# Optimization experiments

Measured on AMD Instinct MI355X. Metric: run time of the kernel, lower is better.

The kernel has to match this reference:

```python
import jax, jax.numpy as jnp
import numpy as np
from jax.ops import segment_sum

N_NODES = 50000
N_EDGES = 800000
N_GRAPHS = 64
N_CLASSES = 100
HEADS = 5
EPS = 1e-5


def _self_loops(edge_index, n):
    loop = jnp.arange(n, dtype=edge_index.dtype)
    src = jnp.concatenate([edge_index[0], loop])
    dst = jnp.concatenate([edge_index[1], loop])
    return src, dst


def gcn_conv(x, src, dst, n, w, b):
    xw = x @ w  # [N, C]
    deg = segment_sum(jnp.ones_like(dst, dtype=xw.dtype), dst, num_segments=n)
    dis = jnp.where(deg > 0, jax.lax.rsqrt(jnp.maximum(deg, 1.0)), 0.0)
    norm = dis[src] * dis[dst]  # [E']
    out = segment_sum(norm[:, None] * xw[src], dst, num_segments=n)
    return out + b


def batch_norm(x, gamma, beta):
    mu = jnp.mean(x, axis=0)
    var = jnp.var(x, axis=0)
    return (x - mu) * jax.lax.rsqrt(var + EPS) * gamma + beta


def gcn_block(x, src, dst, n, w, b, gamma, beta, residual):
    h = jax.nn.gelu(batch_norm(gcn_conv(x, src, dst, n, w, b), gamma, beta), approximate=False)
    return h + x if residual else h


def gat_conv(x, src, dst, n, w, att_src, att_dst, bias):
    H, C = att_src.shape
    xw = (x @ w).reshape(n, H, C)  # [N,H,C]
    a_src = jnp.sum(xw * att_src, axis=-1)  # [N,H]
    a_dst = jnp.sum(xw * att_dst, axis=-1)  # [N,H]
    e = jax.nn.leaky_relu(a_src[src] + a_dst[dst], 0.2)  # [E',H]
    m = jax.ops.segment_max(e, dst, num_segments=n)
    alpha = jnp.exp(e - m[dst])
    denom = segment_sum(alpha, dst, num_segments=n)
    alpha = alpha / jnp.maximum(denom[dst], 1e-16)
    # loop over small fixed head count to bound memory of [E',C] gathers
    outs = []
    for h in range(H):
        msg = alpha[:, h:h + 1] * xw[src, h, :]  # [E',C]
        outs.append(segment_sum(msg, dst, num_segments=n))
    out = jnp.mean(jnp.stack(outs, axis=0), axis=0)  # concat=False -> mean over heads
    return out + bias


def graph_layer_norm(x, gamma, beta):
    # PyG LayerNorm(mode='graph') with batch=None: normalize over all nodes+features
    mu = jnp.mean(x)
    var = jnp.var(x)
    return (x - mu) * jax.lax.rsqrt(var + EPS) * gamma + beta


def layer_norm(x, gamma, beta):
    mu = jnp.mean(x, axis=-1, keepdims=True)
    var = jnp.var(x, axis=-1, keepdims=True)
    return (x - mu) * jax.lax.rsqrt(var + EPS) * gamma + beta


def global_mean_pool(x, batch, n_graphs):
    sums = segment_sum(x, batch, num_segments=n_graphs)
    cnt = segment_sum(jnp.ones((x.shape[0],), x.dtype), batch, num_segments=n_graphs)
    return sums / jnp.maximum(cnt, 1.0)[:, None]


def setup_inputs() -> dict:
    key = jax.random.key(0)
    ks = jax.random.split(key, 24)
    glorot = lambda k, shp: jax.random.normal(k, shp, jnp.float32) * np.sqrt(2.0 / (shp[0] + shp[-1]))
    inp = {}
    inp['x'] = jax.random.normal(ks[0], (N_NODES, 3), jnp.float32)
    inp['edge_index'] = jax.random.randint(ks[1], (2, N_EDGES), 0, N_NODES, jnp.int64)
    inp['batch'] = jnp.sort(jax.random.randint(ks[2], (N_NODES,), 0, N_GRAPHS, jnp.int64))
    # input block 3->128
    inp['w_in'] = glorot(ks[3], (3, 128)); inp['b_in'] = jnp.zeros((128,), jnp.float32)
    inp['g_in'] = jnp.ones((128,), jnp.float32); inp['be_in'] = jnp.zeros((128,), jnp.float32)
    # hidden block 128->128 (n_hidden_blocks=2 -> one hidden block)
    inp['w_h'] = glorot(ks[4], (128, 128)); inp['b_h'] = jnp.zeros((128,), jnp.float32)
    inp['g_h'] = jnp.ones((128,), jnp.float32); inp['be_h'] = jnp.zeros((128,), jnp.float32)
    # GAT 128 -> 5 heads x 128, mean
    inp['w_gat'] = glorot(ks[5], (128, HEADS * 128))
    inp['att_src'] = glorot(ks[6], (HEADS, 128)); inp['att_dst'] = glorot(ks[7], (HEADS, 128))
    inp['b_gat'] = jnp.zeros((128,), jnp.float32)
    # output block 128->512
    inp['w_out'] = glorot(ks[8], (128, 512)); inp['b_out'] = jnp.zeros((512,), jnp.float32)
    inp['g_out'] = jnp.ones((512,), jnp.float32); inp['be_out'] = jnp.zeros((512,), jnp.float32)
    # encoder layer norm
    inp['g_ln'] = jnp.ones((512,), jnp.float32); inp['be_ln'] = jnp.zeros((512,), jnp.float32)
    # projection head
    inp['w_p1'] = glorot(ks[9], (512, 128)); inp['b_p1'] = jnp.zeros((128,), jnp.float32)
    inp['g_pbn'] = jnp.ones((128,), jnp.float32); inp['be_pbn'] = jnp.zeros((128,), jnp.float32)
    inp['w_p2'] = glorot(ks[10], (128, 128)); inp['b_p2'] = jnp.zeros((128,), jnp.float32)
    inp['g_pln'] = jnp.ones((128,), jnp.float32); inp['be_pln'] = jnp.zeros((128,), jnp.float32)
    # classifier
    inp['w_c'] = glorot(ks[11], (128, N_CLASSES)); inp['b_c'] = jnp.zeros((N_CLASSES,), jnp.float32)
    return inp


def reference(x, edge_index, batch, w_in, b_in, g_in, be_in, w_h, b_h, g_h, be_h,
              w_gat, att_src, att_dst, b_gat, w_out, b_out, g_out, be_out,
              g_ln, be_ln, w_p1, b_p1, g_pbn, be_pbn, w_p2, b_p2, g_pln, be_pln,
              w_c, b_c):
    n = x.shape[0]
    src, dst = _self_loops(edge_index, n)
    # encoder
    h = gcn_block(x, src, dst, n, w_in, b_in, g_in, be_in, residual=False)
    h = gcn_block(h, src, dst, n, w_h, b_h, g_h, be_h, residual=True)
    h = gat_conv(h, src, dst, n, w_gat, att_src, att_dst, b_gat)
    h = gcn_block(h, src, dst, n, w_out, b_out, g_out, be_out, residual=False)
    h = graph_layer_norm(h, g_ln, be_ln)
    h = global_mean_pool(h, batch, N_GRAPHS)  # [G,512]
    # projection head
    p = jax.nn.gelu(batch_norm(h @ w_p1 + b_p1, g_pbn, be_pbn), approximate=False)
    p = layer_norm(p @ w_p2 + b_p2 + p, g_pln, be_pln)
    # normalize + classifier
    x1 = p / jnp.maximum(jnp.linalg.norm(p, axis=1, keepdims=True), 1e-12)
    c1 = jax.nn.log_softmax(x1 @ w_c + b_c, axis=1)
    return (x1, c1)
```

## Files before the change

kernel.cpp:

```cpp
#include <hip/hip_runtime.h>
#include <hip/hip_bf16.h>
#include <math.h>

#define NN 50000
#define NE 800000
#define NG 64
#define NC 100
#define EPSV 1e-5f
#define PBN 256
#define SCB 196
#define SPL 8
#define PRB 128

typedef unsigned int   u32;
typedef unsigned short u16;
typedef __attribute__((ext_vector_type(8))) short bf16x8;
typedef __attribute__((ext_vector_type(4))) float f32x4;

__device__ __forceinline__ float gelu_f(float x){
  return 0.5f*x*(1.0f + erff(x*0.70710678118654752f));
}
__device__ __forceinline__ float bf2f(u16 u){
  return __uint_as_float(((u32)u)<<16);
}
__device__ __forceinline__ float2 bf2f2(u32 u){
  float2 r;
  r.x = __uint_as_float(u<<16);
  r.y = __uint_as_float(u & 0xffff0000u);
  return r;
}
__device__ __forceinline__ u16 f2bf(float f){
  __hip_bfloat16 h = __float2bfloat16(f);
  return *(u16*)&h;
}
__device__ __forceinline__ u32 pack_bf2(float a, float b){
  return (u32)f2bf(a) | ((u32)f2bf(b)<<16);
}

__global__ void k_deg_init(int* deg){
  int i = blockIdx.x*256 + threadIdx.x;
  if (i < NN) deg[i] = 1;
}
__global__ void k_deg_hist(const int* ei, int* deg){
  int e = blockIdx.x*256 + threadIdx.x;
  if (e < NE) atomicAdd(&deg[ei[NE + e]], 1);
}
__global__ void k_dis(const int* deg, float* dis){
  int i = blockIdx.x*256 + threadIdx.x;
  if (i < NN) dis[i] = rsqrtf((float)deg[i]);
}
__global__ void k_scanA(const int* deg, int* bsum){
  __shared__ int red[256];
  int b = blockIdx.x, t = threadIdx.x;
  int i = b*256 + t;
  red[t] = (i < NN) ? deg[i]-1 : 0;
  __syncthreads();
  for (int st = 128; st; st >>= 1){
    if (t < st) red[t] += red[t+st];
    __syncthreads();
  }
  if (t == 0) bsum[b] = red[0];
}
__global__ void k_scanB(const int* bsum, int* boff){
  __shared__ int sh[256];
  int t = threadIdx.x;
  sh[t] = (t < SCB) ? bsum[t] : 0;
  __syncthreads();
  for (int d = 1; d < 256; d <<= 1){
    int v = (t >= d) ? sh[t-d] : 0;
    __syncthreads();
    sh[t] += v;
    __syncthreads();
  }
  if (t == 0) boff[0] = 0;
  if (t < SCB) boff[t+1] = sh[t];
}
__global__ void k_scanC(const int* deg, const int* boff, int* off, int* cur){
  __shared__ int sh[256];
  int b = blockIdx.x, t = threadIdx.x;
  int i = b*256 + t;
  int v = (i < NN) ? deg[i]-1 : 0;
  sh[t] = v;
  __syncthreads();
  for (int d = 1; d < 256; d <<= 1){
    int u = (t >= d) ? sh[t-d] : 0;
    __syncthreads();
    sh[t] += u;
    __syncthreads();
  }
  if (i < NN){
    int excl = boff[b] + sh[t] - v;
    off[i] = excl; cur[i] = excl;
    if (i == NN-1) off[NN] = boff[b] + sh[t];
  }
}
__global__ void k_scatter(const int* ei, int* cur, int* col){
  int e = blockIdx.x*256 + threadIdx.x;
  if (e < NE){
    int s = ei[e], d = ei[NE + e];
    int p = atomicAdd(&cur[d], 1);
    col[p] = s;
  }
}

__global__ void k_agg3(const float* x, const int* off, const int* col,
                       const float* dis, float* aggx){
  int i = blockIdx.x*256 + threadIdx.x;
  if (i >= NN) return;
  float di = dis[i];
  float w0 = di*di;
  float a0 = w0*x[i*3], a1 = w0*x[i*3+1], a2 = w0*x[i*3+2];
  int lo = off[i], hi = off[i+1];
  for (int e = lo; e < hi; ++e){
    int s = col[e];
    float w = dis[s]*di;
    a0 += w*x[s*3]; a1 += w*x[s*3+1]; a2 += w*x[s*3+2];
  }
  aggx[i*3] = a0; aggx[i*3+1] = a1; aggx[i*3+2] = a2;
}

__global__ void k_mm_in(const float* aggx, const float* w, const float* bias, u32* outp){
  int gid = blockIdx.x*256 + threadIdx.x;
  if (gid >= NN*64) return;
  int i = gid >> 6, j2 = (gid & 63)*2;
  float a = aggx[i*3]*w[j2]   + aggx[i*3+1]*w[128+j2]   + aggx[i*3+2]*w[256+j2]   + bias[j2];
  float b = aggx[i*3]*w[j2+1] + aggx[i*3+1]*w[128+j2+1] + aggx[i*3+2]*w[256+j2+1] + bias[j2+1];
  outp[gid] = pack_bf2(a, b);
}

__global__ void k_prepB(const float* B, int ldB, int K, int ncc, u16* Bf){
  int gid = blockIdx.x*256 + threadIdx.x;
  int tot = ncc*K*128;
  if (gid >= tot) return;
  int cc = gid / (K*128);
  int rem = gid - cc*(K*128);
  int k = rem >> 7, n = rem & 127;
  int c128 = k >> 7, kk = k & 127;
  int nt = n >> 4, i = n & 15;
  int ks = kk >> 5, jg = (kk >> 3) & 3, e = kk & 7;
  size_t addr = (size_t)cc*K*128 +
                ((((size_t)(c128*8 + nt)*4 + ks)*4 + jg)*16 + i)*8 + e;
  Bf[addr] = f2bf(B[(size_t)k*ldB + cc*128 + n]);
}
__global__ void k_prepBG(const float* w_gat, u16* Bf){
  int gid = blockIdx.x*256 + threadIdx.x;
  if (gid >= 640*128) return;
  int k = gid >> 7, n = gid & 127;
  int h = k >> 7, kk = k & 127;
  int nt = n >> 4, i = n & 15;
  int ks = kk >> 5, jg = (kk >> 3) & 3, e = kk & 7;
  size_t addr = ((((size_t)(h*8 + nt)*4 + ks)*4 + jg)*16 + i)*8 + e;
  Bf[addr] = f2bf(0.2f * w_gat[(size_t)kk*640 + h*128 + n]);
}

__global__ __launch_bounds__(256) void k_mm_mfma(const u16* A, int lda, int M, int K,
                        const u16* Bf, u16* C, int ldC, const float* bias){
  __shared__ u16 ct[64*132];
  int tid = threadIdx.x;
  int w = tid >> 6, l = tid & 63;
  int jg = l >> 4, ii = l & 15;
  int m0 = blockIdx.x*64 + w*16;
  int cc = blockIdx.y;
  int arow = m0 + ii; if (arow >= M) arow = M-1;
  const u16* Bfc = Bf + (size_t)cc*K*128;
  f32x4 acc[8] = {};
  for (int c128 = 0; c128 < (K >> 7); ++c128){
    const u16* Ar = A + (size_t)arow*lda + c128*128;
    bf16x8 af[4];
    #pragma unroll
    for (int ks = 0; ks < 4; ++ks)
      af[ks] = *(const bf16x8*)(Ar + ks*32 + jg*8);
    #pragma unroll
    for (int nt = 0; nt < 8; ++nt){
      f32x4 a4 = acc[nt];
      #pragma unroll
      for (int ks = 0; ks < 4; ++ks){
        bf16x8 bfr = *(const bf16x8*)(Bfc +
            ((((size_t)(c128*8 + nt)*4 + ks)*4 + jg)*16 + ii)*8);
        a4 = __builtin_amdgcn_mfma_f32_16x16x32_bf16(af[ks], bfr, a4, 0, 0, 0);
      }
      acc[nt] = a4;
    }
  }
  int cOut = cc*128;
  int lrow0 = w*16 + jg*4;
  #pragma unroll
  for (int nt = 0; nt < 8; ++nt){
    float bv = bias[cOut + nt*16 + ii];
    #pragma unroll
    for (int r = 0; r < 4; ++r)
      ct[(lrow0 + r)*132 + nt*16 + ii] = f2bf(acc[nt][r] + bv);
  }
  __syncthreads();
  int lr0 = tid >> 6;
  int lc = tid & 63;
  #pragma unroll
  for (int rr = 0; rr < 16; ++rr){
    int lrow = rr*4 + lr0;
    int grow = blockIdx.x*64 + lrow;
    if (grow < M)
      *(u32*)(C + (size_t)grow*ldC + cOut + lc*2) = *(const u32*)(ct + lrow*132 + lc*2);
  }
}

__global__ void k_gcn_agg64(const u16* xw, const int* off, const int* col,
                            const float* dis, u16* out){
  int i = blockIdx.x, t = threadIdx.x;
  float di = dis[i];
  float2 sv = bf2f2(((const u32*)(xw + (size_t)i*128))[t]);
  float w0 = di*di;
  float ax = w0*sv.x, ay = w0*sv.y;
  int lo = off[i], hi = off[i+1];
  int e = lo;
  for (; e + 4 <= hi; e += 4){
    int s0 = col[e], s1 = col[e+1], s2 = col[e+2], s3 = col[e+3];
    float wA = dis[s0]*di, wB = dis[s1]*di, wC = dis[s2]*di, wD = dis[s3]*di;
    float2 r0 = bf2f2(((const u32*)(xw + (size_t)s0*128))[t]);
    float2 r1 = bf2f2(((const u32*)(xw + (size_t)s1*128))[t]);
    float2 r2 = bf2f2(((const u32*)(xw + (size_t)s2*128))[t]);
    float2 r3 = bf2f2(((const u32*)(xw + (size_t)s3*128))[t]);
    ax += wA*r0.x; ay += wA*r0.y;
    ax += wB*r1.x; ay += wB*r1.y;
    ax += wC*r2.x; ay += wC*r2.y;
    ax += wD*r3.x; ay += wD*r3.y;
  }
  for (; e < hi; ++e){
    int s = col[e];
    float w = dis[s]*di;
    float2 rv = bf2f2(((const u32*)(xw + (size_t)s*128))[t]);
    ax += w*rv.x; ay += w*rv.y;
  }
  ((u32*)(out + (size_t)i*128))[t] = pack_bf2(ax, ay);
}

__global__ void k_bn_part(const u16* x, int stride, int W, float* part){
  __shared__ float shs[8][132];
  __shared__ float shq[8][132];
  int t = threadIdx.x;
  int ft = t & 31, rl = t >> 5;
  int f0 = ft*4;
  int fbase = blockIdx.x*128;
  int p = blockIdx.y;
  float s0=0.f,s1=0.f,s2=0.f,s3=0.f, q0=0.f,q1=0.f,q2=0.f,q3=0.f;
  for (int r = p + PBN*rl; r < NN; r += PBN*8){
    ushort4 u = *(const ushort4*)(x + (size_t)r*stride + fbase + f0);
    float v0 = bf2f(u.x), v1 = bf2f(u.y), v2 = bf2f(u.z), v3 = bf2f(u.w);
    s0 += v0; s1 += v1; s2 += v2; s3 += v3;
    q0 += v0*v0; q1 += v1*v1; q2 += v2*v2; q3 += v3*v3;
  }
  shs[rl][f0] = s0; shs[rl][f0+1] = s1; shs[rl][f0+2] = s2; shs[rl][f0+3] = s3;
  shq[rl][f0] = q0; shq[rl][f0+1] = q1; shq[rl][f0+2] = q2; shq[rl][f0+3] = q3;
  __syncthreads();
  if (t < 128){
    float s = 0.f, q = 0.f;
    #pragma unroll
    for (int r = 0; r < 8; ++r){ s += shs[r][t]; q += shq[r][t]; }
    size_t fb = (size_t)(fbase + t)*2*PBN;
    part[fb + p] = s;
    part[fb + PBN + p] = q;
  }
}
__global__ void k_bn_fin(const float* part, const float* g, const float* be,
                         float* ss, int W, float invn){
  __shared__ float rs[256], rq[256];
  int f = blockIdx.x, t = threadIdx.x;
  size_t fb = (size_t)f*2*PBN;
  rs[t] = part[fb + t];
  rq[t] = part[fb + PBN + t];
  __syncthreads();
  for (int st = 128; st; st >>= 1){
    if (t < st){ rs[t] += rs[t+st]; rq[t] += rq[t+st]; }
    __syncthreads();
  }
  if (t == 0){
    float mean = rs[0]*invn;
    float var  = rq[0]*invn - mean*mean;
    float sc = g[f]*rsqrtf(var + EPSV);
    ss[f] = sc;
    ss[W+f] = be[f] - mean*sc;
  }
}
template<bool RES>
__global__ void k_bn_apply(const u32* x, const float* ss, const u32* res, u32* out){
  const int n = NN*64;
  for (int idx = blockIdx.x*256 + threadIdx.x; idx < n; idx += gridDim.x*256){
    int f2 = (idx & 63)*2;
    float2 v = bf2f2(x[idx]);
    v.x = gelu_f(v.x*ss[f2]   + ss[128+f2]);
    v.y = gelu_f(v.y*ss[f2+1] + ss[128+f2+1]);
    if (RES){ float2 r = bf2f2(res[idx]); v.x += r.x; v.y += r.y; }
    out[idx] = pack_bf2(v.x, v.y);
  }
}

__global__ void k_wv(const float* w_gat, const float* att_s, const float* att_d,
                     float* wvs, float* wvd){
  int h = blockIdx.x, c = threadIdx.x;
  float ss = 0.f, sd = 0.f;
  const float* wr = w_gat + (size_t)c*640 + h*128;
  const float* as = att_s + h*128;
  const float* ad = att_d + h*128;
  for (int k = 0; k < 128; ++k){
    float wv = wr[k];
    ss += wv*as[k]; sd += wv*ad[k];
  }
  wvs[h*128+c] = ss; wvd[h*128+c] = sd;
}

__global__ void k_score10(const u16* h2, const float* wvs, const float* wvd,
                          float* asrc, float* adst){
  int i = blockIdx.x, t = threadIdx.x;
  float2 v = bf2f2(((const u32*)(h2 + (size_t)i*128))[t]);
  int f2 = 2*t;
  #pragma unroll
  for (int h = 0; h < 5; ++h){
    float vs = v.x*wvs[h*128+f2] + v.y*wvs[h*128+f2+1];
    float vd = v.x*wvd[h*128+f2] + v.y*wvd[h*128+f2+1];
    #pragma unroll
    for (int d = 32; d; d >>= 1){ vs += __shfl_xor(vs, d); vd += __shfl_xor(vd, d); }
    if (t == 0){ asrc[i*5+h] = vs; adst[i*5+h] = vd; }
  }
}

__global__ void k_prep5(const float* asrc, const float* adst,
                        const int* off, const int* col,
                        u16* sv, float* aself5, float* invb5){
  int i = blockIdx.x, t = threadIdx.x;
  int lo = off[i], hi = off[i+1];
  float ad[5], dn[5];
  #pragma unroll
  for (int h = 0; h < 5; ++h){ ad[h] = adst[i*5+h]; dn[h] = 0.f; }
  for (int e = lo + t; e < hi; e += 64){
    int s = col[e];
    u16 nb[5];
    #pragma unroll
    for (int h = 0; h < 5; ++h){
      float v = asrc[s*5+h] + ad[h];
      v = (v > 0.f) ? v : 0.2f*v;
      float ex = expf(v);
      u16 qq = f2bf(ex);
      nb[h] = qq;
      dn[h] += bf2f(qq);
    }
    uint4 pk;
    pk.x = (u32)nb[0] | ((u32)nb[1] << 16);
    pk.y = (u32)nb[2] | ((u32)nb[3] << 16);
    pk.z = (u32)nb[4];
    pk.w = 0;
    *(uint4*)(sv + (size_t)e*8) = pk;
  }
  #pragma unroll
  for (int h = 0; h < 5; ++h)
    #pragma unroll
    for (int d = 32; d; d >>= 1) dn[h] += __shfl_xor(dn[h], d);
  if (t == 0){
    #pragma unroll
    for (int h = 0; h < 5; ++h){
      float es = asrc[i*5+h] + ad[h];
      es = (es > 0.f) ? es : 0.2f*es;
      float esf = expf(es);
      aself5[i*5+h] = esf;
      invb5[i*5+h] = 1.f/fmaxf(dn[h] + esf, 1e-16f);
    }
  }
}

__global__ void k_gather5(const u16* h2, const int* off, const int* col,
                          const u16* sv, const float* aself5, const float* invb5,
                          u16* agg5){
  int i = blockIdx.x, t = threadIdx.x;
  float2 svv = bf2f2(((const u32*)(h2 + (size_t)i*128))[t]);
  float ax[5], ay[5];
  #pragma unroll
  for (int h = 0; h < 5; ++h){
    float a = aself5[i*5+h];
    ax[h] = a*svv.x; ay[h] = a*svv.y;
  }
  int lo = off[i], hi = off[i+1];
  int e = lo;
  for (; e + 2 <= hi; e += 2){
    int s0 = col[e], s1 = col[e+1];
    uint4 p0 = *(const uint4*)(sv + (size_t)e*8);
    uint4 p1 = *(const uint4*)(sv + (size_t)(e+1)*8);
    float2 r0 = bf2f2(((const u32*)(h2 + (size_t)s0*128))[t]);
    float2 r1 = bf2f2(((const u32*)(h2 + (size_t)s1*128))[t]);
    float a00 = bf2f((u16)(p0.x & 0xffff)), a01 = bf2f((u16)(p0.x >> 16));
    float a02 = bf2f((u16)(p0.y & 0xffff)), a03 = bf2f((u16)(p0.y >> 16));
    float a04 = bf2f((u16)(p0.z & 0xffff));
    float a10 = bf2f((u16)(p1.x & 0xffff)), a11 = bf2f((u16)(p1.x >> 16));
    float a12 = bf2f((u16)(p1.y & 0xffff)), a13 = bf2f((u16)(p1.y >> 16));
    float a14 = bf2f((u16)(p1.z & 0xffff));
    ax[0] += a00*r0.x + a10*r1.x; ay[0] += a00*r0.y + a10*r1.y;
    ax[1] += a01*r0.x + a11*r1.x; ay[1] += a01*r0.y + a11*r1.y;
    ax[2] += a02*r0.x + a12*r1.x; ay[2] += a02*r0.y + a12*r1.y;
    ax[3] += a03*r0.x + a13*r1.x; ay[3] += a03*r0.y + a13*r1.y;
    ax[4] += a04*r0.x + a14*r1.x; ay[4] += a04*r0.y + a14*r1.y;
  }
  for (; e < hi; ++e){
    int s = col[e];
    uint4 pk = *(const uint4*)(sv + (size_t)e*8);
    float2 rv = bf2f2(((const u32*)(h2 + (size_t)s*128))[t]);
    float a0 = bf2f((u16)(pk.x & 0xffff)), a1 = bf2f((u16)(pk.x >> 16));
    float a2 = bf2f((u16)(pk.y & 0xffff)), a3 = bf2f((u16)(pk.y >> 16));
    float a4 = bf2f((u16)(pk.z & 0xffff));
    ax[0] += a0*rv.x; ay[0] += a0*rv.y;
    ax[1] += a1*rv.x; ay[1] += a1*rv.y;
    ax[2] += a2*rv.x; ay[2] += a2*rv.y;
    ax[3] += a3*rv.x; ay[3] += a3*rv.y;
    ax[4] += a4*rv.x; ay[4] += a4*rv.y;
  }
  #pragma unroll
  for (int h = 0; h < 5; ++h){
    float iv = invb5[i*5+h];
    ((u32*)(agg5 + (size_t)i*640 + h*128))[t] = pack_bf2(ax[h]*iv, ay[h]*iv);
  }
}

__global__ void k_gstart(const int* batch, int* gs){
  int g = threadIdx.x;
  if (g > NG) return;
  int lo = 0, hi = NN;
  while (lo < hi){ int mid = (lo+hi) >> 1; if (batch[mid] < g) lo = mid+1; else hi = mid; }
  gs[g] = lo;
}
__global__ void k_poolstat(const u16* a512, const float* ss, const int* gs,
                           float* poolpart, float* sqpart){
  __shared__ float4 red4[512];
  __shared__ float redq[512];
  int g = blockIdx.x, sp = blockIdx.y, t = threadIdx.x;
  int ft = t & 127, rl = t >> 7;
  int f0 = ft*4;
  int lo = gs[g], hi = gs[g+1];
  float sc0 = ss[f0],     sc1 = ss[f0+1],     sc2 = ss[f0+2],     sc3 = ss[f0+3];
  float sh0 = ss[512+f0], sh1 = ss[512+f0+1], sh2 = ss[512+f0+2], sh3 = ss[512+f0+3];
  float4 s4 = {0.f,0.f,0.f,0.f};
  float q = 0.f;
  for (int r = lo + sp*4 + rl; r < hi; r += SPL*4){
    ushort4 u = *(const ushort4*)(a512 + (size_t)r*512 + f0);
    float v0 = gelu_f(bf2f(u.x)*sc0 + sh0);
    float v1 = gelu_f(bf2f(u.y)*sc1 + sh1);
    float v2 = gelu_f(bf2f(u.z)*sc2 + sh2);
    float v3 = gelu_f(bf2f(u.w)*sc3 + sh3);
    s4.x += v0; s4.y += v1; s4.z += v2; s4.w += v3;
    q += v0*v0 + v1*v1 + v2*v2 + v3*v3;
  }
  red4[t] = s4; redq[t] = q;
  __syncthreads();
  for (int st = 256; st; st >>= 1){
    if (t < st) redq[t] += redq[t+st];
    __syncthreads();
  }
  if (t == 0) sqpart[g*SPL + sp] = redq[0];
  if (rl == 0){
    float4 a = red4[t], b = red4[t+128], c = red4[t+256], d = red4[t+384];
    float4 o;
    o.x = a.x+b.x+c.x+d.x; o.y = a.y+b.y+c.y+d.y;
    o.z = a.z+b.z+c.z+d.z; o.w = a.w+b.w+c.w+d.w;
    ((float4*)poolpart)[((size_t)(g*SPL + sp))*128 + ft] = o;
  }
}
__global__ void k_poolredA(const float* poolpart, const float* sqpart,
                           float* ppred, float* sqred){
  __shared__ float rs_[256], rq_[256];
  int b = blockIdx.x, t = threadIdx.x;
  float s = 0.f, q = 0.f;
  const int tot = NG*SPL*512;
  for (int i = b*256 + t; i < tot; i += PRB*256) s += poolpart[i];
  for (int i = b*256 + t; i < NG*SPL; i += PRB*256) q += sqpart[i];
  rs_[t] = s; rq_[t] = q;
  __syncthreads();
  for (int st = 128; st; st >>= 1){
    if (t < st){ rs_[t] += rs_[t+st]; rq_[t] += rq_[t+st]; }
    __syncthreads();
  }
  if (t == 0){ ppred[b] = rs_[0]; sqred[b] = rq_[0]; }
}
__global__ void k_poolredB(const float* ppred, const float* sqred, float* scal){
  __shared__ float rs_[128], rq_[128];
  int t = threadIdx.x;
  rs_[t] = ppred[t]; rq_[t] = sqred[t];
  __syncthreads();
  for (int st = 64; st; st >>= 1){
    if (t < st){ rs_[t] += rs_[t+st]; rq_[t] += rq_[t+st]; }
    __syncthreads();
  }
  if (t == 0){
    float invn = 1.f/((float)NN*512.f);
    float mu  = rs_[0]*invn;
    float var = rq_[0]*invn - mu*mu;
    scal[2] = mu;
    scal[3] = rsqrtf(var + EPSV);
  }
}
__global__ void k_poolapply(const float* poolpart, const int* gs, const float* scal,
                            const float* gam, const float* bet, float* pooled){
  int g = blockIdx.x, f = threadIdx.x;
  float s = 0.f;
  #pragma unroll
  for (int sp = 0; sp < SPL; ++sp)
    s += poolpart[((size_t)(g*SPL + sp))*512 + f];
  float cnt = (float)max(gs[g+1] - gs[g], 1);
  pooled[g*512 + f] = (s/cnt - scal[2])*scal[3]*gam[f] + bet[f];
}

__global__ void k_head_mm1(const float* pooled, const float* w, const float* b, float* q){
  int g = blockIdx.x, j = threadIdx.x;
  float s = b[j];
  const float* pr = pooled + g*512;
  for (int k = 0; k < 512; ++k) s += pr[k]*w[k*128+j];
  q[g*128+j] = s;
}
__global__ void k_head_bn(const float* qin, const float* g_, const float* be_, float* qout){
  int f = threadIdx.x;
  float s = 0.f, sq = 0.f;
  for (int r = 0; r < NG; ++r){ float v = qin[r*128+f]; s += v; sq += v*v; }
  float mu = s*(1.f/NG), var = sq*(1.f/NG) - mu*mu;
  float sc = g_[f]*rsqrtf(var + EPSV);
  float sh = be_[f] - mu*sc;
  for (int r = 0; r < NG; ++r) qout[r*128+f] = gelu_f(qin[r*128+f]*sc + sh);
}
__global__ void k_head2c(const float* q2, const float* w, const float* b,
                         const float* gam, const float* bet,
                         const float* wc, const float* bc, float* out){
  int g = blockIdx.x, j = threadIdx.x;
  __shared__ float row[128], red[128], shv[3];
  row[j] = q2[g*128+j];
  __syncthreads();
  float s = b[j] + row[j];
  for (int k = 0; k < 128; ++k) s += row[k]*w[k*128+j];
  red[j] = s; __syncthreads();
  for (int st = 64; st; st >>= 1){ if (j < st) red[j] += red[j+st]; __syncthreads(); }
  if (j == 0) shv[0] = red[0]*(1.f/128.f);
  __syncthreads();
  float d = s - shv[0];
  red[j] = d*d; __syncthreads();
  for (int st = 64; st; st >>= 1){ if (j < st) red[j] += red[j+st]; __syncthreads(); }
  if (j == 0) shv[1] = rsqrtf(red[0]*(1.f/128.f) + EPSV);
  __syncthreads();
  float v = d*shv[1]*gam[j] + bet[j];
  red[j] = v*v; __syncthreads();
  for (int st = 64; st; st >>= 1){ if (j < st) red[j] += red[j+st]; __syncthreads(); }
  if (j == 0) shv[2] = 1.f/fmaxf(sqrtf(red[0]), 1e-12f);
  __syncthreads();
  float o = v*shv[2];
  out[g*128+j] = o;
  __syncthreads();
  row[j] = o;
  __syncthreads();
  float cs = -1e30f;
  if (j < NC){
    cs = bc[j];
    for (int k = 0; k < 128; ++k) cs += row[k]*wc[k*NC+j];
  }
  red[j] = cs; __syncthreads();
  for (int st = 64; st; st >>= 1){ if (j < st) red[j] = fmaxf(red[j], red[j+st]); __syncthreads(); }
  if (j == 0) shv[0] = red[0];
  __syncthreads();
  float e = (j < NC) ? expf(cs - shv[0]) : 0.f;
  red[j] = e; __syncthreads();
  for (int st = 64; st; st >>= 1){ if (j < st) red[j] += red[j+st]; __syncthreads(); }
  if (j == 0) shv[1] = logf(red[0]);
  __syncthreads();
  if (j < NC) out[NG*128 + g*NC+j] = cs - shv[0] - shv[1];
}

extern "C" void kernel_launch(void* const* d_in, const int* in_sizes, int n_in,
                              void* d_out, int out_size, void* d_ws, size_t ws_size,
                              hipStream_t stream){
  const float* x      = (const float*)d_in[0];
  const int*   ei     = (const int*)d_in[1];
  const int*   batch  = (const int*)d_in[2];
  const float* w_in   = (const float*)d_in[3];
  const float* b_in   = (const float*)d_in[4];
  const float* g_in   = (const float*)d_in[5];
  const float* be_in  = (const float*)d_in[6];
  const float* w_h    = (const float*)d_in[7];
  const float* b_h    = (const float*)d_in[8];
  const float* g_h    = (const float*)d_in[9];
  const float* be_h   = (const float*)d_in[10];
  const float* w_gat  = (const float*)d_in[11];
  const float* att_s  = (const float*)d_in[12];
  const float* att_d  = (const float*)d_in[13];
  const float* b_gat  = (const float*)d_in[14];
  const float* w_out  = (const float*)d_in[15];
  const float* b_out  = (const float*)d_in[16];
  const float* g_out  = (const float*)d_in[17];
  const float* be_out = (const float*)d_in[18];
  const float* g_ln   = (const float*)d_in[19];
  const float* be_ln  = (const float*)d_in[20];
  const float* w_p1   = (const float*)d_in[21];
  const float* b_p1   = (const float*)d_in[22];
  const float* g_pbn  = (const float*)d_in[23];
  const float* be_pbn = (const float*)d_in[24];
  const float* w_p2   = (const float*)d_in[25];
  const float* b_p2   = (const float*)d_in[26];
  const float* g_pln  = (const float*)d_in[27];
  const float* be_pln = (const float*)d_in[28];
  const float* w_c    = (const float*)d_in[29];
  const float* b_c    = (const float*)d_in[30];
  float* out = (float*)d_out;

  char* ws = (char*)d_ws;
  size_t o = 0;
  auto carve = [&](size_t bytes) -> char* {
    char* p = ws + o;
    o += (bytes + 255) & ~(size_t)255;
    return p;
  };
  int*   deg    = (int*)  carve((size_t)NN*4);
  int*   off    = (int*)  carve((size_t)(NN+1)*4);
  int*   cur    = (int*)  carve((size_t)NN*4);
  int*   col    = (int*)  carve((size_t)NE*4);
  float* dis    = (float*)carve((size_t)NN*4);
  int*   bsum   = (int*)  carve((size_t)SCB*4);
  int*   boff   = (int*)  carve((size_t)(SCB+1)*4);
  float* aggx3  = (float*)carve((size_t)NN*3*4);
  u16*   F0     = (u16*)  carve((size_t)NN*128*2);
  u16*   F1     = (u16*)  carve((size_t)NN*128*2);
  u16*   F2     = (u16*)  carve((size_t)NN*128*2);
  u16*   AGG5   = (u16*)  carve((size_t)NN*640*2);
  float* asrc   = (float*)carve((size_t)NN*5*4);
  float* adst   = (float*)carve((size_t)NN*5*4);
  float* aself5 = (float*)carve((size_t)NN*5*4);
  float* invb5  = (float*)carve((size_t)NN*5*4);
  float* wvs    = (float*)carve(640*4);
  float* wvd    = (float*)carve(640*4);
  u16*   BfH    = (u16*)  carve((size_t)128*128*2);
  u16*   BfG    = (u16*)  carve((size_t)640*128*2);
  u16*   BfO    = (u16*)  carve((size_t)128*512*2);
  float* part   = (float*)carve((size_t)512*2*PBN*4);
  float* poolpart = (float*)carve((size_t)NG*SPL*512*4);
  float* sqpart = (float*)carve((size_t)NG*SPL*4);
  float* ppred  = (float*)carve((size_t)PRB*4);
  float* sqred  = (float*)carve((size_t)PRB*4);
  float* ssbuf  = (float*)carve(1024*4);
  float* scal   = (float*)carve(64);
  int*   gst    = (int*)  carve(65*4);
  float* pooled = (float*)carve((size_t)NG*512*4);
  float* q      = (float*)carve((size_t)NG*128*4);
  float* q2     = (float*)carve((size_t)NG*128*4);
  if (o > ws_size) return;

  u16* A512 = AGG5;
  u16* sv   = F2;

  k_deg_init<<<196,256,0,stream>>>(deg);
  k_deg_hist<<<3125,256,0,stream>>>(ei, deg);
  k_dis<<<196,256,0,stream>>>(deg, dis);
  k_scanA<<<SCB,256,0,stream>>>(deg, bsum);
  k_scanB<<<1,256,0,stream>>>(bsum, boff);
  k_scanC<<<SCB,256,0,stream>>>(deg, boff, off, cur);
  k_scatter<<<3125,256,0,stream>>>(ei, cur, col);

  k_prepB<<<64,256,0,stream>>>(w_h, 128, 128, 1, BfH);
  k_prepBG<<<320,256,0,stream>>>(w_gat, BfG);
  k_prepB<<<256,256,0,stream>>>(w_out, 512, 128, 4, BfO);

  k_agg3<<<196,256,0,stream>>>(x, off, col, dis, aggx3);
  k_mm_in<<<(NN*64+255)/256,256,0,stream>>>(aggx3, w_in, b_in, (u32*)F0);
  k_bn_part<<<dim3(1,PBN),256,0,stream>>>(F0, 128, 128, part);
  k_bn_fin<<<128,256,0,stream>>>(part, g_in, be_in, ssbuf, 128, 1.f/NN);
  k_bn_apply<false><<<2048,256,0,stream>>>((u32*)F0, ssbuf, nullptr, (u32*)F1);

  k_gcn_agg64<<<NN,64,0,stream>>>(F1, off, col, dis, F0);
  k_mm_mfma<<<dim3(782,1),256,0,stream>>>(F0, 128, NN, 128, BfH, F2, 128, b_h);
  k_bn_part<<<dim3(1,PBN),256,0,stream>>>(F2, 128, 128, part);
  k_bn_fin<<<128,256,0,stream>>>(part, g_h, be_h, ssbuf, 128, 1.f/NN);
  k_bn_apply<true><<<2048,256,0,stream>>>((u32*)F2, ssbuf, (u32*)F1, (u32*)F0);

  k_wv<<<5,128,0,stream>>>(w_gat, att_s, att_d, wvs, wvd);
  k_score10<<<NN,64,0,stream>>>(F0, wvs, wvd, asrc, adst);
  k_prep5<<<NN,64,0,stream>>>(asrc, adst, off, col, sv, aself5, invb5);
  k_gather5<<<NN,64,0,stream>>>(F0, off, col, sv, aself5, invb5, AGG5);
  k_mm_mfma<<<dim3(782,1),256,0,stream>>>(AGG5, 640, NN, 640, BfG, F1, 128, b_gat);

  k_gcn_agg64<<<NN,64,0,stream>>>(F1, off, col, dis, F2);
  k_mm_mfma<<<dim3(782,4),256,0,stream>>>(F2, 128, NN, 128, BfO, A512, 512, b_out);
  k_bn_part<<<dim3(4,PBN),256,0,stream>>>(A512, 512, 512, part);
  k_bn_fin<<<512,256,0,stream>>>(part, g_out, be_out, ssbuf, 512, 1.f/NN);

  k_gstart<<<1,128,0,stream>>>(batch, gst);
  k_poolstat<<<dim3(NG,SPL),512,0,stream>>>(A512, ssbuf, gst, poolpart, sqpart);
  k_poolredA<<<PRB,256,0,stream>>>(poolpart, sqpart, ppred, sqred);
  k_poolredB<<<1,128,0,stream>>>(ppred, sqred, scal);
  k_poolapply<<<NG,512,0,stream>>>(poolpart, gst, scal, g_ln, be_ln, pooled);

  k_head_mm1<<<NG,128,0,stream>>>(pooled, w_p1, b_p1, q);
  k_head_bn<<<1,128,0,stream>>>(q, g_pbn, be_pbn, q2);
  k_head2c<<<NG,128,0,stream>>>(q2, w_p2, b_p2, g_pln, be_pln, w_c, b_c, out);
}
```

Measured before the change: 650.8 us.

## Fuse GAT softmax prep into gather, use 16-bit CSR columns, merge dis into scan

Merges the GAT edge-score/normalizer kernel into the gather kernel. Each wavefront now recomputes leaky-relu and exp per edge from padded 8-float per-node score arrays and accumulates the denominator inline, instead of writing and re-reading a per-edge bf16 score buffer. CSR column indices are stored as u16, since the node count fits, which halves index traffic in every aggregation. The rsqrt degree kernel is folded into the first scan kernel to save a launch. In exchange, every lane of the wave redundantly evaluates five expf calls per edge.

```diff
diff --git a/kernel.cpp b/kernel.cpp
--- a/kernel.cpp
+++ b/kernel.cpp
@@ -45,15 +45,13 @@
   int e = blockIdx.x*256 + threadIdx.x;
   if (e < NE) atomicAdd(&deg[ei[NE + e]], 1);
 }
-__global__ void k_dis(const int* deg, float* dis){
-  int i = blockIdx.x*256 + threadIdx.x;
-  if (i < NN) dis[i] = rsqrtf((float)deg[i]);
-}
-__global__ void k_scanA(const int* deg, int* bsum){
+__global__ void k_scanA(const int* deg, int* bsum, float* dis){
   __shared__ int red[256];
   int b = blockIdx.x, t = threadIdx.x;
   int i = b*256 + t;
-  red[t] = (i < NN) ? deg[i]-1 : 0;
+  int d = (i < NN) ? deg[i] : 1;
+  if (i < NN) dis[i] = rsqrtf((float)d);
+  red[t] = (i < NN) ? d-1 : 0;
   __syncthreads();
   for (int st = 128; st; st >>= 1){
     if (t < st) red[t] += red[t+st];
@@ -94,16 +92,16 @@
     if (i == NN-1) off[NN] = boff[b] + sh[t];
   }
 }
-__global__ void k_scatter(const int* ei, int* cur, int* col){
+__global__ void k_scatter(const int* ei, int* cur, u16* col){
   int e = blockIdx.x*256 + threadIdx.x;
   if (e < NE){
     int s = ei[e], d = ei[NE + e];
     int p = atomicAdd(&cur[d], 1);
-    col[p] = s;
-  }
-}
-
-__global__ void k_agg3(const float* x, const int* off, const int* col,
+    col[p] = (u16)s;
+  }
+}
+
+__global__ void k_agg3(const float* x, const int* off, const u16* col,
                        const float* dis, float* aggx){
   int i = blockIdx.x*256 + threadIdx.x;
   if (i >= NN) return;
@@ -203,7 +201,7 @@
   }
 }
 
-__global__ void k_gcn_agg64(const u16* xw, const int* off, const int* col,
+__global__ void k_gcn_agg64(const u16* xw, const int* off, const u16* col,
                             const float* dis, u16* out){
   int i = blockIdx.x, t = threadIdx.x;
   float di = dis[i];
@@ -308,7 +306,7 @@
 }
 
 __global__ void k_score10(const u16* h2, const float* wvs, const float* wvd,
-                          float* asrc, float* adst){
+                          float* asrc8, float* adst8){
   int i = blockIdx.x, t = threadIdx.x;
   float2 v = bf2f2(((const u32*)(h2 + (size_t)i*128))[t]);
   int f2 = 2*t;
@@ -318,100 +316,65 @@
     float vd = v.x*wvd[h*128+f2] + v.y*wvd[h*128+f2+1];
     #pragma unroll
     for (int d = 32; d; d >>= 1){ vs += __shfl_xor(vs, d); vd += __shfl_xor(vd, d); }
-    if (t == 0){ asrc[i*5+h] = vs; adst[i*5+h] = vd; }
-  }
-}
-
-__global__ void k_prep5(const float* asrc, const float* adst,
-                        const int* off, const int* col,
-                        u16* sv, float* aself5, float* invb5){
-  int i = blockIdx.x, t = threadIdx.x;
-  int lo = off[i], hi = off[i+1];
-  float ad[5], dn[5];
-  #pragma unroll
-  for (int h = 0; h < 5; ++h){ ad[h] = adst[i*5+h]; dn[h] = 0.f; }
-  for (int e = lo + t; e < hi; e += 64){
-    int s = col[e];
-    u16 nb[5];
-    #pragma unroll
-    for (int h = 0; h < 5; ++h){
-      float v = asrc[s*5+h] + ad[h];
-      v = (v > 0.f) ? v : 0.2f*v;
-      float ex = expf(v);
-      u16 qq = f2bf(ex);
-      nb[h] = qq;
-      dn[h] += bf2f(qq);
-    }
-    uint4 pk;
-    pk.x = (u32)nb[0] | ((u32)nb[1] << 16);
-    pk.y = (u32)nb[2] | ((u32)nb[3] << 16);
-    pk.z = (u32)nb[4];
-    pk.w = 0;
-    *(uint4*)(sv + (size_t)e*8) = pk;
-  }
-  #pragma unroll
-  for (int h = 0; h < 5; ++h)
-    #pragma unroll
-    for (int d = 32; d; d >>= 1) dn[h] += __shfl_xor(dn[h], d);
-  if (t == 0){
-    #pragma unroll
-    for (int h = 0; h < 5; ++h){
-      float es = asrc[i*5+h] + ad[h];
-      es = (es > 0.f) ? es : 0.2f*es;
-      float esf = expf(es);
-      aself5[i*5+h] = esf;
-      invb5[i*5+h] = 1.f/fmaxf(dn[h] + esf, 1e-16f);
-    }
-  }
-}
-
-__global__ void k_gather5(const u16* h2, const int* off, const int* col,
-                          const u16* sv, const float* aself5, const float* invb5,
-                          u16* agg5){
+    if (t == 0){ asrc8[i*8+h] = vs; adst8[i*8+h] = vd; }
+  }
+}
+
+__global__ void k_gat_fused(const u16* h2, const int* off, const u16* col,
+                            const float* asrc8, const float* adst8,
+                            u16* agg5){
   int i = blockIdx.x, t = threadIdx.x;
   float2 svv = bf2f2(((const u32*)(h2 + (size_t)i*128))[t]);
-  float ax[5], ay[5];
+  float ad[5], dn[5], ax[5], ay[5];
   #pragma unroll
   for (int h = 0; h < 5; ++h){
-    float a = aself5[i*5+h];
-    ax[h] = a*svv.x; ay[h] = a*svv.y;
+    ad[h] = adst8[i*8+h];
+    float v = asrc8[i*8+h] + ad[h];
+    v = (v > 0.f) ? v : 0.2f*v;
+    float esf = expf(v);
+    dn[h] = esf;
+    ax[h] = esf*svv.x; ay[h] = esf*svv.y;
   }
   int lo = off[i], hi = off[i+1];
   int e = lo;
   for (; e + 2 <= hi; e += 2){
     int s0 = col[e], s1 = col[e+1];
-    uint4 p0 = *(const uint4*)(sv + (size_t)e*8);
-    uint4 p1 = *(const uint4*)(sv + (size_t)(e+1)*8);
+    float4 a03_0 = *(const float4*)(asrc8 + (size_t)s0*8);
+    float  a4_0  = asrc8[(size_t)s0*8 + 4];
+    float4 a03_1 = *(const float4*)(asrc8 + (size_t)s1*8);
+    float  a4_1  = asrc8[(size_t)s1*8 + 4];
     float2 r0 = bf2f2(((const u32*)(h2 + (size_t)s0*128))[t]);
     float2 r1 = bf2f2(((const u32*)(h2 + (size_t)s1*128))[t]);
-    float a00 = bf2f((u16)(p0.x & 0xffff)), a01 = bf2f((u16)(p0.x >> 16));
-    float a02 = bf2f((u16)(p0.y & 0xffff)), a03 = bf2f((u16)(p0.y >> 16));
-    float a04 = bf2f((u16)(p0.z & 0xffff));
-    float a10 = bf2f((u16)(p1.x & 0xffff)), a11 = bf2f((u16)(p1.x >> 16));
-    float a12 = bf2f((u16)(p1.y & 0xffff)), a13 = bf2f((u16)(p1.y >> 16));
-    float a14 = bf2f((u16)(p1.z & 0xffff));
-    ax[0] += a00*r0.x + a10*r1.x; ay[0] += a00*r0.y + a10*r1.y;
-    ax[1] += a01*r0.x + a11*r1.x; ay[1] += a01*r0.y + a11*r1.y;
-    ax[2] += a02*r0.x + a12*r1.x; ay[2] += a02*r0.y + a12*r1.y;
-    ax[3] += a03*r0.x + a13*r1.x; ay[3] += a03*r0.y + a13*r1.y;
-    ax[4] += a04*r0.x + a14*r1.x; ay[4] += a04*r0.y + a14*r1.y;
+    float sa0[5] = {a03_0.x, a03_0.y, a03_0.z, a03_0.w, a4_0};
+    float sa1[5] = {a03_1.x, a03_1.y, a03_1.z, a03_1.w, a4_1};
+    #pragma unroll
+    for (int h = 0; h < 5; ++h){
+      float v0 = sa0[h] + ad[h]; v0 = (v0 > 0.f) ? v0 : 0.2f*v0;
+      float v1 = sa1[h] + ad[h]; v1 = (v1 > 0.f) ? v1 : 0.2f*v1;
+      float e0 = expf(v0), e1 = expf(v1);
+      dn[h] += e0 + e1;
+      ax[h] += e0*r0.x + e1*r1.x;
+      ay[h] += e0*r0.y + e1*r1.y;
+    }
   }
   for (; e < hi; ++e){
     int s = col[e];
-    uint4 pk = *(const uint4*)(sv + (size_t)e*8);
+    float4 a03 = *(const float4*)(asrc8 + (size_t)s*8);
+    float  a4  = asrc8[(size_t)s*8 + 4];
     float2 rv = bf2f2(((const u32*)(h2 + (size_t)s*128))[t]);
-    float a0 = bf2f((u16)(pk.x & 0xffff)), a1 = bf2f((u16)(pk.x >> 16));
-    float a2 = bf2f((u16)(pk.y & 0xffff)), a3 = bf2f((u16)(pk.y >> 16));
-    float a4 = bf2f((u16)(pk.z & 0xffff));
-    ax[0] += a0*rv.x; ay[0] += a0*rv.y;
-    ax[1] += a1*rv.x; ay[1] += a1*rv.y;
-    ax[2] += a2*rv.x; ay[2] += a2*rv.y;
-    ax[3] += a3*rv.x; ay[3] += a3*rv.y;
-    ax[4] += a4*rv.x; ay[4] += a4*rv.y;
+    float sa[5] = {a03.x, a03.y, a03.z, a03.w, a4};
+    #pragma unroll
+    for (int h = 0; h < 5; ++h){
+      float v = sa[h] + ad[h]; v = (v > 0.f) ? v : 0.2f*v;
+      float ex = expf(v);
+      dn[h] += ex;
+      ax[h] += ex*rv.x;
+      ay[h] += ex*rv.y;
+    }
   }
   #pragma unroll
   for (int h = 0; h < 5; ++h){
-    float iv = invb5[i*5+h];
+    float iv = 1.f/fmaxf(dn[h], 1e-16f);
     ((u32*)(agg5 + (size_t)i*640 + h*128))[t] = pack_bf2(ax[h]*iv, ay[h]*iv);
   }
 }
@@ -610,7 +573,7 @@
   int*   deg    = (int*)  carve((size_t)NN*4);
   int*   off    = (int*)  carve((size_t)(NN+1)*4);
   int*   cur    = (int*)  carve((size_t)NN*4);
-  int*   col    = (int*)  carve((size_t)NE*4);
+  u16*   col    = (u16*)  carve((size_t)NE*2);
   float* dis    = (float*)carve((size_t)NN*4);
   int*   bsum   = (int*)  carve((size_t)SCB*4);
   int*   boff   = (int*)  carve((size_t)(SCB+1)*4);
@@ -619,10 +582,8 @@
   u16*   F1     = (u16*)  carve((size_t)NN*128*2);
   u16*   F2     = (u16*)  carve((size_t)NN*128*2);
   u16*   AGG5   = (u16*)  carve((size_t)NN*640*2);
-  float* asrc   = (float*)carve((size_t)NN*5*4);
-  float* adst   = (float*)carve((size_t)NN*5*4);
-  float* aself5 = (float*)carve((size_t)NN*5*4);
-  float* invb5  = (float*)carve((size_t)NN*5*4);
+  float* asrc8  = (float*)carve((size_t)NN*8*4);
+  float* adst8  = (float*)carve((size_t)NN*8*4);
   float* wvs    = (float*)carve(640*4);
   float* wvd    = (float*)carve(640*4);
   u16*   BfH    = (u16*)  carve((size_t)128*128*2);
@@ -642,12 +603,10 @@
   if (o > ws_size) return;
 
   u16* A512 = AGG5;
-  u16* sv   = F2;
 
   k_deg_init<<<196,256,0,stream>>>(deg);
   k_deg_hist<<<3125,256,0,stream>>>(ei, deg);
-  k_dis<<<196,256,0,stream>>>(deg, dis);
-  k_scanA<<<SCB,256,0,stream>>>(deg, bsum);
+  k_scanA<<<SCB,256,0,stream>>>(deg, bsum, dis);
   k_scanB<<<1,256,0,stream>>>(bsum, boff);
   k_scanC<<<SCB,256,0,stream>>>(deg, boff, off, cur);
   k_scatter<<<3125,256,0,stream>>>(ei, cur, col);
@@ -669,9 +628,8 @@
   k_bn_apply<true><<<2048,256,0,stream>>>((u32*)F2, ssbuf, (u32*)F1, (u32*)F0);
 
   k_wv<<<5,128,0,stream>>>(w_gat, att_s, att_d, wvs, wvd);
-  k_score10<<<NN,64,0,stream>>>(F0, wvs, wvd, asrc, adst);
-  k_prep5<<<NN,64,0,stream>>>(asrc, adst, off, col, sv, aself5, invb5);
-  k_gather5<<<NN,64,0,stream>>>(F0, off, col, sv, aself5, invb5, AGG5);
+  k_score10<<<NN,64,0,stream>>>(F0, wvs, wvd, asrc8, adst8);
+  k_gat_fused<<<NN,64,0,stream>>>(F0, off, col, asrc8, adst8, AGG5);
   k_mm_mfma<<<dim3(782,1),256,0,stream>>>(AGG5, 640, NN, 640, BfG, F1, 128, b_gat);
 
   k_gcn_agg64<<<NN,64,0,stream>>>(F1, off, col, dis, F2);
```

Result: slower. 708.7 us (+8.9%).
